# Kernel optimization log

Hardware: AMD Instinct MI355X
Metric: run time of the kernel (lower is better)

The kernel has to match this reference:

```python
import jax, jax.numpy as jnp
import numpy as np

N = 50000      # nodes
E = 800000     # edges (before self-loops)
D_IN = 256     # input feature dim
H = 4          # attention heads
C = 32         # per-head channels
HID = H * C    # 128, concat output dim
BN_EPS = 1e-5


def setup_inputs() -> dict:
    key = jax.random.key(0)
    ks = jax.random.split(key, 24)
    inp = {}
    inp["x"] = jax.random.normal(ks[0], (N, D_IN), jnp.float32)
    inp["edge_index"] = jax.random.randint(ks[1], (2, E), 0, N, jnp.int32)
    # layer 1 GATConv params
    inp["W1"] = jax.random.normal(ks[2], (D_IN, HID), jnp.float32) * (2.0 / (D_IN + HID)) ** 0.5
    inp["att_src1"] = jax.random.normal(ks[3], (H, C), jnp.float32) * 0.1
    inp["att_dst1"] = jax.random.normal(ks[4], (H, C), jnp.float32) * 0.1
    inp["bias1"] = jnp.zeros((HID,), jnp.float32)
    # layer 1 BatchNorm (eval mode)
    inp["gamma1"] = 1.0 + 0.1 * jax.random.normal(ks[5], (HID,), jnp.float32)
    inp["beta1"] = 0.1 * jax.random.normal(ks[6], (HID,), jnp.float32)
    inp["mean1"] = 0.1 * jax.random.normal(ks[7], (HID,), jnp.float32)
    inp["var1"] = 0.5 + jax.random.uniform(ks[8], (HID,), jnp.float32)
    # layer 2 GATConv params
    inp["W2"] = jax.random.normal(ks[9], (HID, HID), jnp.float32) * (2.0 / (HID + HID)) ** 0.5
    inp["att_src2"] = jax.random.normal(ks[10], (H, C), jnp.float32) * 0.1
    inp["att_dst2"] = jax.random.normal(ks[11], (H, C), jnp.float32) * 0.1
    inp["bias2"] = jnp.zeros((HID,), jnp.float32)
    # layer 2 BatchNorm (eval mode)
    inp["gamma2"] = 1.0 + 0.1 * jax.random.normal(ks[12], (HID,), jnp.float32)
    inp["beta2"] = 0.1 * jax.random.normal(ks[13], (HID,), jnp.float32)
    inp["mean2"] = 0.1 * jax.random.normal(ks[14], (HID,), jnp.float32)
    inp["var2"] = 0.5 + jax.random.uniform(ks[15], (HID,), jnp.float32)
    return inp


def _gat_layer(x, src, dst, W, att_src, att_dst, bias):
    # x: [N, D]; src/dst: [Etot] with self-loops already appended
    h = (x @ W).reshape(N, H, C)                       # [N, H, C]
    a_s = jnp.einsum("nhc,hc->nh", h, att_src)         # [N, H]
    a_d = jnp.einsum("nhc,hc->nh", h, att_dst)         # [N, H]
    e = jax.nn.leaky_relu(a_s[src] + a_d[dst], 0.2)    # [Etot, H]
    # edge softmax over incoming edges of each destination node
    m = jax.ops.segment_max(e, dst, num_segments=N)    # [N, H]
    ex = jnp.exp(e - m[dst])                           # [Etot, H]
    den = jax.ops.segment_sum(ex, dst, num_segments=N) # [N, H]
    alpha = ex / (den[dst] + 1e-16)                    # [Etot, H]
    out = jax.ops.segment_sum(h[src] * alpha[:, :, None], dst, num_segments=N)
    return out.reshape(N, HID) + bias                  # concat heads + bias


def _bn_eval(x, gamma, beta, mean, var):
    return (x - mean) * (gamma * jax.lax.rsqrt(var + BN_EPS)) + beta


def reference(x, edge_index, W1, att_src1, att_dst1, bias1, gamma1, beta1, mean1, var1,
              W2, att_src2, att_dst2, bias2, gamma2, beta2, mean2, var2):
    loop = jnp.arange(N, dtype=edge_index.dtype)
    src = jnp.concatenate([edge_index[0], loop])  # PyG GATConv adds self-loops
    dst = jnp.concatenate([edge_index[1], loop])
    h = _gat_layer(x, src, dst, W1, att_src1, att_dst1, bias1)
    h = jax.nn.relu(_bn_eval(h, gamma1, beta1, mean1, var1))  # dropout = identity (eval)
    h = _gat_layer(h, src, dst, W2, att_src2, att_dst2, bias2)
    h = jax.nn.relu(_bn_eval(h, gamma2, beta2, mean2, var2))
    return h
```

## Files before the change

kernel.cpp:

```cpp
#include <hip/hip_runtime.h>
#include <math.h>

#define N_NODES 50000
#define EDGES   800000
#define ETOT    (EDGES + N_NODES)
#define HID     128
#define NH      4

typedef __attribute__((ext_vector_type(8))) short short8;
typedef __attribute__((ext_vector_type(4))) float floatx4;

__device__ inline unsigned short f2bf(float f) {
    unsigned int u = __float_as_uint(f);
    u = u + 0x7FFFu + ((u >> 16) & 1u);
    return (unsigned short)(u >> 16);
}

#define NB 391
#define BCAP 2688
#define CHUNK 4096
#define BIN_BLOCKS ((ETOT + CHUNK - 1) / CHUNK)
#define G1A 391
#define NSPLIT 25024
#define NSPLIT4 6256

__device__ __forceinline__ void bin_scatter_body(int* histL, int bid,
                                                 const int* __restrict__ ei,
                                                 int* __restrict__ cursor,
                                                 int* __restrict__ binned) {
    int t = threadIdx.x;
    for (int b = t; b < NB; b += 256) histL[b] = 0;
    __syncthreads();
    int base = bid * CHUNK;
#pragma unroll
    for (int j = 0; j < 16; j++) {
        int e = base + j * 256 + t;
        if (e < ETOT) {
            int d = (e < EDGES) ? ei[EDGES + e] : (e - EDGES);
            atomicAdd(&histL[d >> 7], 1);
        }
    }
    __syncthreads();
    for (int b = t; b < NB; b += 256) {
        int c = histL[b];
        histL[b] = c ? (b * BCAP + atomicAdd(&cursor[b], c)) : 0;
    }
    __syncthreads();
#pragma unroll
    for (int j = 0; j < 16; j++) {
        int e = base + j * 256 + t;
        if (e < ETOT) {
            int s, d;
            if (e < EDGES) { s = ei[e]; d = ei[EDGES + e]; }
            else           { s = d = e - EDGES; }
            int bb = d >> 7;
            int pos = atomicAdd(&histL[bb], 1);
            if (pos < (bb + 1) * BCAP)
                binned[pos] = (s << 7) | (d & 127);
        }
    }
}

__device__ __forceinline__ void bin_finalize_body(int* histN, int* excl, int b,
                                                  const int* __restrict__ binned,
                                                  const int* __restrict__ cursor,
                                                  int* __restrict__ starts,
                                                  int* __restrict__ degs,
                                                  int* __restrict__ csr) {
    int t = threadIdx.x;
    int n0 = b << 7;
    int S = b * BCAP;
    int cnt = cursor[b];
    if (cnt > BCAP) cnt = BCAP;
    if (t < 128) histN[t] = 0;
    __syncthreads();
    for (int j = t; j < cnt; j += 256)
        atomicAdd(&histN[binned[S + j] & 127], 1);
    __syncthreads();
    int v = (t < 128) ? histN[t] : 0;
    if (t < 128) excl[t] = v;
    __syncthreads();
    for (int off = 1; off < 128; off <<= 1) {
        int x = 0, add = 0;
        if (t < 128) { x = excl[t]; if (t >= off) add = excl[t - off]; }
        __syncthreads();
        if (t < 128) excl[t] = x + add;
        __syncthreads();
    }
    if (t < 128) {
        int ex = excl[t] - v;
        int n = n0 + t;
        if (n < N_NODES) { starts[n] = S + ex; degs[n] = v; }
        histN[t] = ex;
    }
    __syncthreads();
    for (int j = t; j < cnt; j += 256) {
        int e = binned[S + j];
        int pos = atomicAdd(&histN[e & 127], 1);
        csr[S + pos] = e >> 7;
    }
}

__global__ void wtrans_coef_kernel(const float* __restrict__ W1, const float* __restrict__ W2,
                                   unsigned short* __restrict__ Wt1, unsigned short* __restrict__ Wt2,
                                   const float* __restrict__ b1, const float* __restrict__ g1,
                                   const float* __restrict__ be1, const float* __restrict__ mn1,
                                   const float* __restrict__ vr1,
                                   const float* __restrict__ b2, const float* __restrict__ g2,
                                   const float* __restrict__ be2, const float* __restrict__ mn2,
                                   const float* __restrict__ vr2, float* __restrict__ coef,
                                   int* __restrict__ cursor) {
    int i = blockIdx.x * 256 + threadIdx.x;
    if (i < NB) cursor[i] = 0;
    if (i < 256 * 128) { int k = i >> 7, n = i & 127; Wt1[n * 256 + k] = f2bf(W1[i]); }
    if (i < 128 * 128) { int k = i >> 7, n = i & 127; Wt2[n * 128 + k] = f2bf(W2[i]); }
    if (blockIdx.x == 0) {
        int t = threadIdx.x;
        if (t < 128) {
            float sc = g1[t] * rsqrtf(vr1[t] + 1e-5f);
            coef[t]       = sc;
            coef[128 + t] = be1[t] + (b1[t] - mn1[t]) * sc;
        } else {
            int c = t - 128;
            float sc = g2[c] * rsqrtf(vr2[c] + 1e-5f);
            coef[256 + c] = sc;
            coef[384 + c] = be2[c] + (b2[c] - mn2[c]) * sc;
        }
    }
}

#define GR   64
#define KC   64
#define PADK 88
#define PADH 136

union Smem {
    struct { unsigned short Xs[GR][PADK]; unsigned short Ws[HID][PADK]; } s;
    unsigned short Hs[GR][PADH];
};

template<bool XBF16>
__device__ __forceinline__ void gemm_att_body(Smem& sm, int bid,
                                              const void* Xv,
                                              const unsigned short* Wt,
                                              const float* att_src,
                                              const float* att_dst,
                                              unsigned short* Hout,
                                              float* aS, float* aD, int K) {
    int t = threadIdx.x, lane = t & 63, w = t >> 6;
    int quad = lane >> 4, nl = lane & 15;
    int rowBase = bid * GR;

    floatx4 acc[8];
    floatx4 zero = {0.f, 0.f, 0.f, 0.f};
#pragma unroll
    for (int b = 0; b < 8; b++) acc[b] = zero;

    const float*          Xf = (const float*)Xv;
    const unsigned short* Xb = (const unsigned short*)Xv;

    for (int k0 = 0; k0 < K; k0 += KC) {
#pragma unroll
        for (int it = 0; it < 2; it++) {
            int s5 = t + it * 256;
            int row = s5 >> 3, kg = s5 & 7;
            int gr = rowBase + row;
            unsigned short tmp[8];
            if (XBF16) {
                uint4 v = make_uint4(0, 0, 0, 0);
                if (gr < N_NODES) v = *(const uint4*)&Xb[(unsigned)(gr * K + k0 + kg * 8)];
                *(uint4*)tmp = v;
            } else {
                float4 v0 = make_float4(0, 0, 0, 0), v1 = v0;
                if (gr < N_NODES) {
                    const float* p = &Xf[(unsigned)(gr * K + k0 + kg * 8)];
                    v0 = *(const float4*)p;
                    v1 = *(const float4*)(p + 4);
                }
                tmp[0] = f2bf(v0.x); tmp[1] = f2bf(v0.y); tmp[2] = f2bf(v0.z); tmp[3] = f2bf(v0.w);
                tmp[4] = f2bf(v1.x); tmp[5] = f2bf(v1.y); tmp[6] = f2bf(v1.z); tmp[7] = f2bf(v1.w);
            }
            *(uint4*)&sm.s.Xs[row][kg * 8] = *(uint4*)tmp;
        }
#pragma unroll
        for (int it = 0; it < 4; it++) {
            int s5 = t + it * 256;
            int n = s5 >> 3, kg = s5 & 7;
            *(uint4*)&sm.s.Ws[n][kg * 8] = *(const uint4*)&Wt[(unsigned)(n * K + k0 + kg * 8)];
        }
        __syncthreads();
#pragma unroll
        for (int ks = 0; ks < 2; ks++) {
            int kb = ks * 32 + quad * 8;
            short8 a0 = *(const short8*)&sm.s.Xs[w * 16 + nl][kb];
#pragma unroll
            for (int ct = 0; ct < 8; ct++) {
                short8 b = *(const short8*)&sm.s.Ws[ct * 16 + nl][kb];
                acc[ct] = __builtin_amdgcn_mfma_f32_16x16x32_bf16(a0, b, acc[ct], 0, 0, 0);
            }
        }
        __syncthreads();
    }

#pragma unroll
    for (int ct = 0; ct < 8; ct++)
#pragma unroll
        for (int r = 0; r < 4; r++)
            sm.Hs[w * 16 + quad * 4 + r][ct * 16 + nl] = f2bf(acc[ct][r]);

    float asv[8], adv[8];
    {
        const float* ap = &att_src[nl * 8];
        const float* dp = &att_dst[nl * 8];
        *(float4*)&asv[0] = *(const float4*)ap;  *(float4*)&asv[4] = *(const float4*)(ap + 4);
        *(float4*)&adv[0] = *(const float4*)dp;  *(float4*)&adv[4] = *(const float4*)(dp + 4);
    }
    int hd = nl >> 2;
#pragma unroll
    for (int it = 0; it < 4; it++) {
        int rl = w * 16 + it * 4 + quad;
        int grow = rowBase + rl;
        uint4 v = *(const uint4*)&sm.Hs[rl][nl * 8];
        float f[8];
        f[0] = __uint_as_float(v.x << 16); f[1] = __uint_as_float(v.x & 0xffff0000u);
        f[2] = __uint_as_float(v.y << 16); f[3] = __uint_as_float(v.y & 0xffff0000u);
        f[4] = __uint_as_float(v.z << 16); f[5] = __uint_as_float(v.z & 0xffff0000u);
        f[6] = __uint_as_float(v.w << 16); f[7] = __uint_as_float(v.w & 0xffff0000u);
        float ds = 0.f, dd = 0.f;
#pragma unroll
        for (int j = 0; j < 8; j++) {
            ds = fmaf(f[j], asv[j], ds);
            dd = fmaf(f[j], adv[j], dd);
        }
        ds += __shfl_xor(ds, 1); ds += __shfl_xor(ds, 2);
        dd += __shfl_xor(dd, 1); dd += __shfl_xor(dd, 2);
        if (grow < N_NODES) {
            *(uint4*)&Hout[(unsigned)(grow * HID + nl * 8)] = v;
            if ((nl & 3) == 0) { aS[grow * 4 + hd] = ds; aD[grow * 4 + hd] = dd; }
        }
    }
}

#define ECAP 64

__device__ __forceinline__ void prefetchR(uint4 (&buf)[4], int sregr, const char* hbase,
                                          int sBase, int l16b) {
#pragma unroll
    for (int u = 0; u < 4; u++) {
        int se = __builtin_amdgcn_ds_bpermute(sBase | (u << 2), sregr);
        buf[u] = *(const uint4*)(hbase + (((long)se) << 8) + l16b);
    }
}

__device__ __forceinline__ void consumeR(const uint4 (&buf)[4], float xrr, int aBase,
                                         float (&acc)[8]) {
#pragma unroll
    for (int u = 0; u < 4; u++) {
        float au = __uint_as_float((unsigned)__builtin_amdgcn_ds_bpermute(
                        aBase | (u << 2), (int)__float_as_uint(xrr)));
        uint4 v = buf[u];
        acc[0] = fmaf(__uint_as_float(v.x << 16),         au, acc[0]);
        acc[1] = fmaf(__uint_as_float(v.x & 0xffff0000u), au, acc[1]);
        acc[2] = fmaf(__uint_as_float(v.y << 16),         au, acc[2]);
        acc[3] = fmaf(__uint_as_float(v.y & 0xffff0000u), au, acc[3]);
        acc[4] = fmaf(__uint_as_float(v.z << 16),         au, acc[4]);
        acc[5] = fmaf(__uint_as_float(v.z & 0xffff0000u), au, acc[5]);
        acc[6] = fmaf(__uint_as_float(v.w << 16),         au, acc[6]);
        acc[7] = fmaf(__uint_as_float(v.w & 0xffff0000u), au, acc[7]);
    }
}

template<bool OUTBF16>
__device__ __forceinline__ void gather_body(int nb,
                                            const unsigned short* hfeat,
                                            const float* a_s, const float* a_d,
                                            const int* starts, const int* degs,
                                            const int* csr,
                                            const float* coefA, const float* coefB,
                                            void* outv) {
    int t = threadIdx.x, lane = t & 63, ws = t >> 6;
    int h = lane >> 4, l16 = lane & 15;
    int n = nb * 4 + ws;
    int start = starts[n];
    int deg = degs[n];
    float adh = a_d[(unsigned)(n * 4 + h)];
    const char* hbase = (const char*)hfeat;
    int sBase = lane & 48;
    int aBase = ((lane & 12) << 4) | sBase;
    int l16b = l16 << 4;

    int sreg[4];
#pragma unroll
    for (int it = 0; it < 4; it++) {
        int j = l16 + it * 16;
        sreg[it] = (j < deg) ? csr[start + j] : 0;
    }
    float e[4];
#pragma unroll
    for (int it = 0; it < 4; it++) {
        int j = l16 + it * 16;
        e[it] = -1e30f;
        if (j < deg) {
            float as = a_s[(unsigned)(sreg[it] * 4 + h)];
            float v = as + adh;
            e[it] = v > 0.f ? v : 0.2f * v;
        }
    }

    int cap = deg < ECAP ? deg : ECAP;
    uint4 vA[4], vB[4];
    prefetchR(vA, sreg[0], hbase, sBase, l16b);
    if (cap > 16) prefetchR(vB, sreg[1], hbase, sBase, l16b);

    float m = fmaxf(fmaxf(e[0], e[1]), fmaxf(e[2], e[3]));
    for (int j = ECAP + l16; j < deg; j += 16) {
        int s = csr[start + j];
        float as = a_s[(unsigned)(s * 4 + h)];
        float v = as + adh; v = v > 0.f ? v : 0.2f * v;
        m = fmaxf(m, v);
    }
#pragma unroll
    for (int off = 1; off < 16; off <<= 1) m = fmaxf(m, __shfl_xor(m, off));

    float x[4];
    float d = 0.f;
#pragma unroll
    for (int it = 0; it < 4; it++) { x[it] = __expf(e[it] - m); d += x[it]; }
    for (int j = ECAP + l16; j < deg; j += 16) {
        int s = csr[start + j];
        float as = a_s[(unsigned)(s * 4 + h)];
        float v = as + adh; v = v > 0.f ? v : 0.2f * v;
        d += __expf(v - m);
    }
#pragma unroll
    for (int off = 1; off < 16; off <<= 1) d += __shfl_xor(d, off);
    float rd = 1.0f / (d + 1e-16f);
    float xr[4];
#pragma unroll
    for (int it = 0; it < 4; it++) xr[it] = x[it] * rd;

    float acc[8];
#pragma unroll
    for (int j = 0; j < 8; j++) acc[j] = 0.f;
    consumeR(vA, xr[0], aBase, acc);
    if (cap > 16) {
        if (cap > 32) prefetchR(vA, sreg[2], hbase, sBase, l16b);
        consumeR(vB, xr[1], aBase, acc);
        if (cap > 32) {
            if (cap > 48) prefetchR(vB, sreg[3], hbase, sBase, l16b);
            consumeR(vA, xr[2], aBase, acc);
            if (cap > 48) consumeR(vB, xr[3], aBase, acc);
        }
    }
    if (deg > ECAP) {
        int hh = l16 >> 2;
        int gB = (lane & 12) << 4;
        float mB  = __uint_as_float((unsigned)__builtin_amdgcn_ds_bpermute(gB, (int)__float_as_uint(m)));
        float rdB = __uint_as_float((unsigned)__builtin_amdgcn_ds_bpermute(gB, (int)__float_as_uint(rd)));
        float adhB = a_d[(unsigned)(n * 4 + hh)];
        for (int j = ECAP; j < deg; j++) {
            int s = csr[start + j];
            float asv = a_s[(unsigned)(s * 4 + hh)];
            float v2 = asv + adhB; v2 = v2 > 0.f ? v2 : 0.2f * v2;
            float al = __expf(v2 - mB) * rdB;
            uint4 v = *(const uint4*)(hbase + (((long)s) << 8) + l16b);
            acc[0] = fmaf(__uint_as_float(v.x << 16),         al, acc[0]);
            acc[1] = fmaf(__uint_as_float(v.x & 0xffff0000u), al, acc[1]);
            acc[2] = fmaf(__uint_as_float(v.y << 16),         al, acc[2]);
            acc[3] = fmaf(__uint_as_float(v.y & 0xffff0000u), al, acc[3]);
            acc[4] = fmaf(__uint_as_float(v.z << 16),         al, acc[4]);
            acc[5] = fmaf(__uint_as_float(v.z & 0xffff0000u), al, acc[5]);
            acc[6] = fmaf(__uint_as_float(v.w << 16),         al, acc[6]);
            acc[7] = fmaf(__uint_as_float(v.w & 0xffff0000u), al, acc[7]);
        }
    }

#pragma unroll
    for (int j = 0; j < 8; j++) {
        acc[j] += __shfl_xor(acc[j], 16);
        acc[j] += __shfl_xor(acc[j], 32);
    }

    int g = lane >> 4;
    float o0 = acc[0], o1 = acc[1];
    if (g == 1) { o0 = acc[2]; o1 = acc[3]; }
    if (g == 2) { o0 = acc[4]; o1 = acc[5]; }
    if (g == 3) { o0 = acc[6]; o1 = acc[7]; }
    int c = (l16 << 3) + (g << 1);
    float2 cA = *(const float2*)&coefA[c];
    float2 cB = *(const float2*)&coefB[c];
    float r0 = fmaxf(fmaf(o0, cA.x, cB.x), 0.f);
    float r1 = fmaxf(fmaf(o1, cA.y, cB.y), 0.f);
    unsigned oidx = (unsigned)(n * 64 + (l16 << 2) + g);
    if (OUTBF16) {
        unsigned int pk = (unsigned int)f2bf(r0) | ((unsigned int)f2bf(r1) << 16);
        ((unsigned int*)outv)[oidx] = pk;
    } else {
        ((float2*)outv)[oidx] = make_float2(r0, r1);
    }
}

__global__ __launch_bounds__(256) void fused_scatter_gemm1a(
        const int* ei, int* cursor, int* binned,
        const float* x, const unsigned short* Wt1,
        const float* att_src, const float* att_dst,
        unsigned short* Hout, float* aS, float* aD) {
    __shared__ Smem sm;
    __shared__ int histL[NB];
    if (blockIdx.x < BIN_BLOCKS) {
        bin_scatter_body(histL, blockIdx.x, ei, cursor, binned);
    } else {
        gemm_att_body<false>(sm, blockIdx.x - BIN_BLOCKS, x, Wt1, att_src, att_dst,
                             Hout, aS, aD, 256);
    }
}

__global__ __launch_bounds__(256) void fused_finalize_gemm1b(
        const int* binned, const int* cursor,
        int* starts, int* degs, int* csr,
        const float* x, const unsigned short* Wt1,
        const float* att_src, const float* att_dst,
        unsigned short* Hout, float* aS, float* aD) {
    __shared__ Smem sm;
    __shared__ int histN[128];
    __shared__ int excl[128];
    if (blockIdx.x < NB) {
        bin_finalize_body(histN, excl, blockIdx.x, binned, cursor, starts, degs, csr);
    } else {
        gemm_att_body<false>(sm, blockIdx.x, x, Wt1, att_src, att_dst,
                             Hout, aS, aD, 256);
    }
}

__global__ __launch_bounds__(256) void fused_gemm2a_gather1b(
        const unsigned short* x2b, const unsigned short* Wt2,
        const float* as2, const float* ad2,
        unsigned short* hbB, float* aS2, float* aD2,
        const unsigned short* hbA, const float* aS1, const float* aD1,
        const int* starts, const int* degs, const int* csr,
        const float* coef1, unsigned short* x2bOut) {
    __shared__ Smem sm;
    if (blockIdx.x < G1A) {
        gemm_att_body<true>(sm, blockIdx.x, x2b, Wt2, as2, ad2, hbB, aS2, aD2, 128);
    } else {
        gather_body<true>(NSPLIT4 + (int)blockIdx.x - G1A, hbA, aS1, aD1,
                          starts, degs, csr, coef1, coef1 + 128, (void*)x2bOut);
    }
}

template<bool XBF16>
__global__ __launch_bounds__(256) void gemm_att_kernel(const void* Xv,
                                                       const unsigned short* Wt,
                                                       const float* att_src,
                                                       const float* att_dst,
                                                       unsigned short* Hout,
                                                       float* aS, float* aD,
                                                       int K, int bidOff) {
    __shared__ Smem sm;
    gemm_att_body<XBF16>(sm, blockIdx.x + bidOff, Xv, Wt, att_src, att_dst, Hout, aS, aD, K);
}

template<bool OUTBF16>
__global__ __launch_bounds__(256) void gather_kernel(const unsigned short* hfeat,
                                                     const float* a_s, const float* a_d,
                                                     const int* starts, const int* degs,
                                                     const int* csr,
                                                     const float* coefA, const float* coefB,
                                                     void* outv, int nbOff) {
    gather_body<OUTBF16>((int)blockIdx.x + nbOff, hfeat, a_s, a_d, starts, degs, csr,
                         coefA, coefB, outv);
}

extern "C" void kernel_launch(void* const* d_in, const int* in_sizes, int n_in,
                              void* d_out, int out_size, void* d_ws, size_t ws_size,
                              hipStream_t stream) {
    const float* x    = (const float*)d_in[0];
    const int*   ei   = (const int*)d_in[1];
    const float* W1   = (const float*)d_in[2];
    const float* as1  = (const float*)d_in[3];
    const float* ad1  = (const float*)d_in[4];
    const float* b1   = (const float*)d_in[5];
    const float* g1   = (const float*)d_in[6];
    const float* be1  = (const float*)d_in[7];
    const float* mn1  = (const float*)d_in[8];
    const float* vr1  = (const float*)d_in[9];
    const float* W2   = (const float*)d_in[10];
    const float* as2  = (const float*)d_in[11];
    const float* ad2  = (const float*)d_in[12];
    const float* b2   = (const float*)d_in[13];
    const float* g2   = (const float*)d_in[14];
    const float* be2  = (const float*)d_in[15];
    const float* mn2  = (const float*)d_in[16];
    const float* vr2  = (const float*)d_in[17];
    float* out = (float*)d_out;

    unsigned short* hbA = (unsigned short*)d_ws;
    unsigned short* x2b = hbA + (size_t)N_NODES * HID;
    unsigned short* Wt1 = x2b + (size_t)N_NODES * HID;
    unsigned short* Wt2 = Wt1 + 128 * 256;
    float* aS1   = (float*)(Wt2 + 128 * 128);
    float* aD1   = aS1 + N_NODES * NH;
    float* aS2   = aD1 + N_NODES * NH;
    float* aD2   = aS2 + N_NODES * NH;
    float* coef  = aD2 + N_NODES * NH;
    int* cursor  = (int*)(coef + 512);
    int* starts  = cursor + 512;
    int* degs    = starts + N_NODES;
    int* csr     = degs + N_NODES;
    int* binned  = csr + NB * BCAP;
    unsigned short* hbB = (unsigned short*)binned;

    size_t need = (size_t)((char*)binned - (char*)d_ws) + (size_t)N_NODES * HID * 2;
    bool big = ws_size >= need;
    if (!big) { hbB = hbA; aS2 = aS1; aD2 = aD1; }

    wtrans_coef_kernel<<<128, 256, 0, stream>>>(W1, W2, Wt1, Wt2,
                                                b1, g1, be1, mn1, vr1,
                                                b2, g2, be2, mn2, vr2, coef, cursor);

    int gemmGrid = (N_NODES + GR - 1) / GR;
    int nodeGrid = N_NODES / 4;

    fused_scatter_gemm1a<<<BIN_BLOCKS + G1A, 256, 0, stream>>>(
        ei, cursor, binned, x, Wt1, as1, ad1, hbA, aS1, aD1);
    fused_finalize_gemm1b<<<gemmGrid, 256, 0, stream>>>(
        binned, cursor, starts, degs, csr, x, Wt1, as1, ad1, hbA, aS1, aD1);

    if (big) {
        gather_kernel<true><<<NSPLIT4, 256, 0, stream>>>(hbA, aS1, aD1, starts, degs, csr,
                                                         coef, coef + 128, (void*)x2b, 0);
        fused_gemm2a_gather1b<<<G1A + (nodeGrid - NSPLIT4), 256, 0, stream>>>(
            x2b, Wt2, as2, ad2, hbB, aS2, aD2,
            hbA, aS1, aD1, starts, degs, csr, coef, x2b);
        gemm_att_kernel<true><<<gemmGrid - G1A, 256, 0, stream>>>(
            x2b, Wt2, as2, ad2, hbB, aS2, aD2, 128, G1A);
        gather_kernel<false><<<nodeGrid, 256, 0, stream>>>(hbB, aS2, aD2, starts, degs, csr,
                                                           coef + 256, coef + 384, (void*)out, 0);
    } else {
        gather_kernel<true><<<nodeGrid, 256, 0, stream>>>(hbA, aS1, aD1, starts, degs, csr,
                                                          coef, coef + 128, (void*)x2b, 0);
        gemm_att_kernel<true><<<gemmGrid, 256, 0, stream>>>(x2b, Wt2, as2, ad2, hbA, aS1, aD1,
                                                            128, 0);
        gather_kernel<false><<<nodeGrid, 256, 0, stream>>>(hbA, aS1, aD1, starts, degs, csr,
                                                           coef + 256, coef + 384, (void*)out, 0);
    }
}
```

Measured before the change: 253.9 us.

## Fuse whole two-layer GAT pipeline into one cooperative persistent kernel with grid syncs

Replaces the chain of separate launches (weight transpose, binning, GEMM, CSR finalize, two gathers, second GEMM) with a single cooperative mega-kernel. Persistent blocks loop over the virtual block IDs of each phase, with grid.sync between phases. The aim is to remove kernel launch gaps and tail idle time between stages. In exchange it drops the hand-tuned overlap of the layer-1 gather with the layer-2 GEMM, and it caps registers through launch_bounds(256,4). It falls back to a simplified multi-launch path when cooperative launch is unavailable.

```diff
diff --git a/kernel.cpp b/kernel.cpp
--- a/kernel.cpp
+++ b/kernel.cpp
@@ -1,5 +1,8 @@
 #include <hip/hip_runtime.h>
+#include <hip/hip_cooperative_groups.h>
 #include <math.h>
+
+namespace cg = cooperative_groups;
 
 #define N_NODES 50000
 #define EDGES   800000
@@ -20,15 +23,14 @@
 #define BCAP 2688
 #define CHUNK 4096
 #define BIN_BLOCKS ((ETOT + CHUNK - 1) / CHUNK)
-#define G1A 391
-#define NSPLIT 25024
-#define NSPLIT4 6256
+#define GEMM_TILES 782
 
 __device__ __forceinline__ void bin_scatter_body(int* histL, int bid,
                                                  const int* __restrict__ ei,
                                                  int* __restrict__ cursor,
                                                  int* __restrict__ binned) {
     int t = threadIdx.x;
+    __syncthreads();
     for (int b = t; b < NB; b += 256) histL[b] = 0;
     __syncthreads();
     int base = bid * CHUNK;
@@ -72,6 +74,7 @@
     int S = b * BCAP;
     int cnt = cursor[b];
     if (cnt > BCAP) cnt = BCAP;
+    __syncthreads();
     if (t < 128) histN[t] = 0;
     __syncthreads();
     for (int j = t; j < cnt; j += 256)
@@ -101,20 +104,17 @@
     }
 }
 
-__global__ void wtrans_coef_kernel(const float* __restrict__ W1, const float* __restrict__ W2,
-                                   unsigned short* __restrict__ Wt1, unsigned short* __restrict__ Wt2,
-                                   const float* __restrict__ b1, const float* __restrict__ g1,
-                                   const float* __restrict__ be1, const float* __restrict__ mn1,
-                                   const float* __restrict__ vr1,
-                                   const float* __restrict__ b2, const float* __restrict__ g2,
-                                   const float* __restrict__ be2, const float* __restrict__ mn2,
-                                   const float* __restrict__ vr2, float* __restrict__ coef,
-                                   int* __restrict__ cursor) {
-    int i = blockIdx.x * 256 + threadIdx.x;
+__device__ __forceinline__ void wtrans_body(int vb,
+        const float* W1, const float* W2,
+        unsigned short* Wt1, unsigned short* Wt2,
+        const float* b1, const float* g1, const float* be1, const float* mn1, const float* vr1,
+        const float* b2, const float* g2, const float* be2, const float* mn2, const float* vr2,
+        float* coef, int* cursor) {
+    int i = vb * 256 + threadIdx.x;
     if (i < NB) cursor[i] = 0;
     if (i < 256 * 128) { int k = i >> 7, n = i & 127; Wt1[n * 256 + k] = f2bf(W1[i]); }
     if (i < 128 * 128) { int k = i >> 7, n = i & 127; Wt2[n * 128 + k] = f2bf(W2[i]); }
-    if (blockIdx.x == 0) {
+    if (vb == 0) {
         int t = threadIdx.x;
         if (t < 128) {
             float sc = g1[t] * rsqrtf(vr1[t] + 1e-5f);
@@ -150,6 +150,8 @@
     int t = threadIdx.x, lane = t & 63, w = t >> 6;
     int quad = lane >> 4, nl = lane & 15;
     int rowBase = bid * GR;
+
+    __syncthreads();
 
     floatx4 acc[8];
     floatx4 zero = {0.f, 0.f, 0.f, 0.f};
@@ -400,6 +402,76 @@
     }
 }
 
+struct MegaArgs {
+    const int* ei; const float* x;
+    const float* W1; const float* W2;
+    const float* as1; const float* ad1;
+    const float* b1; const float* g1; const float* be1; const float* mn1; const float* vr1;
+    const float* as2; const float* ad2;
+    const float* b2; const float* g2; const float* be2; const float* mn2; const float* vr2;
+    unsigned short* Wt1; unsigned short* Wt2;
+    unsigned short* hbA; unsigned short* x2b; unsigned short* hbB;
+    float* aS1; float* aD1; float* aS2; float* aD2;
+    float* coef; int* cursor; int* starts; int* degs; int* binned; int* csr;
+    float* out;
+};
+
+__global__ __launch_bounds__(256, 4) void mega_kernel(MegaArgs a) {
+    cg::grid_group grid = cg::this_grid();
+    __shared__ Smem sm;
+    __shared__ int histL[NB];
+    __shared__ int histN[128];
+    __shared__ int excl[128];
+    int bid = blockIdx.x, G = gridDim.x;
+
+    for (int vb = bid; vb < 128; vb += G)
+        wtrans_body(vb, a.W1, a.W2, a.Wt1, a.Wt2, a.b1, a.g1, a.be1, a.mn1, a.vr1,
+                    a.b2, a.g2, a.be2, a.mn2, a.vr2, a.coef, a.cursor);
+    __threadfence();
+    grid.sync();
+
+    for (int vb = bid; vb < BIN_BLOCKS + GEMM_TILES; vb += G) {
+        if (vb < BIN_BLOCKS)
+            bin_scatter_body(histL, vb, a.ei, a.cursor, a.binned);
+        else
+            gemm_att_body<false>(sm, vb - BIN_BLOCKS, a.x, a.Wt1, a.as1, a.ad1,
+                                 a.hbA, a.aS1, a.aD1, 256);
+    }
+    __threadfence();
+    grid.sync();
+
+    for (int vb = bid; vb < NB; vb += G)
+        bin_finalize_body(histN, excl, vb, a.binned, a.cursor, a.starts, a.degs, a.csr);
+    __threadfence();
+    grid.sync();
+
+    for (int vb = bid; vb < N_NODES / 4; vb += G)
+        gather_body<true>(vb, a.hbA, a.aS1, a.aD1, a.starts, a.degs, a.csr,
+                          a.coef, a.coef + 128, (void*)a.x2b);
+    __threadfence();
+    grid.sync();
+
+    for (int vb = bid; vb < GEMM_TILES; vb += G)
+        gemm_att_body<true>(sm, vb, a.x2b, a.Wt2, a.as2, a.ad2, a.hbB, a.aS2, a.aD2, 128);
+    __threadfence();
+    grid.sync();
+
+    for (int vb = bid; vb < N_NODES / 4; vb += G)
+        gather_body<false>(vb, a.hbB, a.aS2, a.aD2, a.starts, a.degs, a.csr,
+                           a.coef + 256, a.coef + 384, (void*)a.out);
+}
+
+__global__ void wtrans_coef_kernel(const float* W1, const float* W2,
+                                   unsigned short* Wt1, unsigned short* Wt2,
+                                   const float* b1, const float* g1, const float* be1,
+                                   const float* mn1, const float* vr1,
+                                   const float* b2, const float* g2, const float* be2,
+                                   const float* mn2, const float* vr2,
+                                   float* coef, int* cursor) {
+    wtrans_body(blockIdx.x, W1, W2, Wt1, Wt2, b1, g1, be1, mn1, vr1,
+                b2, g2, be2, mn2, vr2, coef, cursor);
+}
+
 __global__ __launch_bounds__(256) void fused_scatter_gemm1a(
         const int* ei, int* cursor, int* binned,
         const float* x, const unsigned short* Wt1,
@@ -432,32 +504,15 @@
     }
 }
 
-__global__ __launch_bounds__(256) void fused_gemm2a_gather1b(
-        const unsigned short* x2b, const unsigned short* Wt2,
-        const float* as2, const float* ad2,
-        unsigned short* hbB, float* aS2, float* aD2,
-        const unsigned short* hbA, const float* aS1, const float* aD1,
-        const int* starts, const int* degs, const int* csr,
-        const float* coef1, unsigned short* x2bOut) {
-    __shared__ Smem sm;
-    if (blockIdx.x < G1A) {
-        gemm_att_body<true>(sm, blockIdx.x, x2b, Wt2, as2, ad2, hbB, aS2, aD2, 128);
-    } else {
-        gather_body<true>(NSPLIT4 + (int)blockIdx.x - G1A, hbA, aS1, aD1,
-                          starts, degs, csr, coef1, coef1 + 128, (void*)x2bOut);
-    }
-}
-
 template<bool XBF16>
 __global__ __launch_bounds__(256) void gemm_att_kernel(const void* Xv,
                                                        const unsigned short* Wt,
                                                        const float* att_src,
                                                        const float* att_dst,
                                                        unsigned short* Hout,
-                                                       float* aS, float* aD,
-                                                       int K, int bidOff) {
+                                                       float* aS, float* aD, int K) {
     __shared__ Smem sm;
-    gemm_att_body<XBF16>(sm, blockIdx.x + bidOff, Xv, Wt, att_src, att_dst, Hout, aS, aD, K);
+    gemm_att_body<XBF16>(sm, blockIdx.x, Xv, Wt, att_src, att_dst, Hout, aS, aD, K);
 }
 
 template<bool OUTBF16>
@@ -466,8 +521,8 @@
                                                      const int* starts, const int* degs,
                                                      const int* csr,
                                                      const float* coefA, const float* coefB,
-                                                     void* outv, int nbOff) {
-    gather_body<OUTBF16>((int)blockIdx.x + nbOff, hfeat, a_s, a_d, starts, degs, csr,
+                                                     void* outv) {
+    gather_body<OUTBF16>((int)blockIdx.x, hfeat, a_s, a_d, starts, degs, csr,
                          coefA, coefB, outv);
 }
 
@@ -514,34 +569,44 @@
     bool big = ws_size >= need;
     if (!big) { hbB = hbA; aS2 = aS1; aD2 = aD1; }
 
+    static int megaGrid = 0;
+    if (megaGrid == 0) {
+        int coop = 0, numCU = 0, blocksPerCU = 0;
+        hipDeviceGetAttribute(&coop, hipDeviceAttributeCooperativeLaunch, 0);
+        hipDeviceGetAttribute(&numCU, hipDeviceAttributeMultiprocessorCount, 0);
+        hipError_t e = hipOccupancyMaxActiveBlocksPerMultiprocessor(
+            &blocksPerCU, (const void*)mega_kernel, 256, 0);
+        if (coop && numCU > 0 && e == hipSuccess && blocksPerCU > 0)
+            megaGrid = blocksPerCU * numCU;
+        else
+            megaGrid = -1;
+    }
+
+    if (megaGrid > 0) {
+        MegaArgs a = { ei, x, W1, W2, as1, ad1, b1, g1, be1, mn1, vr1,
+                       as2, ad2, b2, g2, be2, mn2, vr2,
+                       Wt1, Wt2, hbA, x2b, hbB, aS1, aD1, aS2, aD2,
+                       coef, cursor, starts, degs, binned, csr, out };
+        void* kp[] = { (void*)&a };
+        hipError_t err = hipLaunchCooperativeKernel((const void*)mega_kernel,
+                                                    dim3(megaGrid), dim3(256),
+                                                    kp, 0, stream);
+        if (err == hipSuccess) return;
+        megaGrid = -1;
+    }
+
+    int gemmGrid = GEMM_TILES;
+    int nodeGrid = N_NODES / 4;
     wtrans_coef_kernel<<<128, 256, 0, stream>>>(W1, W2, Wt1, Wt2,
                                                 b1, g1, be1, mn1, vr1,
                                                 b2, g2, be2, mn2, vr2, coef, cursor);
-
-    int gemmGrid = (N_NODES + GR - 1) / GR;
-    int nodeGrid = N_NODES / 4;
-
-    fused_scatter_gemm1a<<<BIN_BLOCKS + G1A, 256, 0, stream>>>(
+    fused_scatter_gemm1a<<<BIN_BLOCKS + NB, 256, 0, stream>>>(
         ei, cursor, binned, x, Wt1, as1, ad1, hbA, aS1, aD1);
     fused_finalize_gemm1b<<<gemmGrid, 256, 0, stream>>>(
         binned, cursor, starts, degs, csr, x, Wt1, as1, ad1, hbA, aS1, aD1);
-
-    if (big) {
-        gather_kernel<true><<<NSPLIT4, 256, 0, stream>>>(hbA, aS1, aD1, starts, degs, csr,
-                                                         coef, coef + 128, (void*)x2b, 0);
-        fused_gemm2a_gather1b<<<G1A + (nodeGrid - NSPLIT4), 256, 0, stream>>>(
-            x2b, Wt2, as2, ad2, hbB, aS2, aD2,
-            hbA, aS1, aD1, starts, degs, csr, coef, x2b);
-        gemm_att_kernel<true><<<gemmGrid - G1A, 256, 0, stream>>>(
-            x2b, Wt2, as2, ad2, hbB, aS2, aD2, 128, G1A);
-        gather_kernel<false><<<nodeGrid, 256, 0, stream>>>(hbB, aS2, aD2, starts, degs, csr,
-                                                           coef + 256, coef + 384, (void*)out, 0);
-    } else {
-        gather_kernel<true><<<nodeGrid, 256, 0, stream>>>(hbA, aS1, aD1, starts, degs, csr,
-                                                          coef, coef + 128, (void*)x2b, 0);
-        gemm_att_kernel<true><<<gemmGrid, 256, 0, stream>>>(x2b, Wt2, as2, ad2, hbA, aS1, aD1,
-                                                            128, 0);
-        gather_kernel<false><<<nodeGrid, 256, 0, stream>>>(hbA, aS1, aD1, starts, degs, csr,
-                                                           coef + 256, coef + 384, (void*)out, 0);
-    }
-}
+    gather_kernel<true><<<nodeGrid, 256, 0, stream>>>(hbA, aS1, aD1, starts, degs, csr,
+                                                      coef, coef + 128, (void*)x2b);
+    gemm_att_kernel<true><<<gemmGrid, 256, 0, stream>>>(x2b, Wt2, as2, ad2, hbB, aS2, aD2, 128);
+    gather_kernel<false><<<nodeGrid, 256, 0, stream>>>(hbB, aS2, aD2, starts, degs, csr,
+                                                       coef + 256, coef + 384, (void*)out);
+}
```

Result: slower. 914.3 us (+260.1%).
